# Kernel tuning notes

Hardware: AMD Instinct MI355X
Metric: run time of the kernel (lower is better)

Reference implementation:

```python
import jax, jax.numpy as jnp
import numpy as np

N, E, D, L, B, T = 50000, 600000, 128, 7, 512, 10
ATOM_DIMS = [119, 4, 12, 12, 10, 6, 6, 2, 2]
BOND_DIMS = [5, 6, 2]
MSG_EPS = 1e-7   # GENConv message epsilon
BN_EPS = 1e-5    # torch BatchNorm1d eps


def _offsets(dims):
    return jnp.asarray(np.concatenate([[0], np.cumsum(dims[:-1])]), dtype=jnp.int32)


def setup_inputs():
    key = jax.random.key(0)
    k = lambda i: jax.random.fold_in(key, i)
    x = jnp.stack([jax.random.randint(k(i), (N,), 0, d) for i, d in enumerate(ATOM_DIMS)], axis=1)
    edge_attr = jnp.stack([jax.random.randint(k(100 + i), (E,), 0, d) for i, d in enumerate(BOND_DIMS)], axis=1)
    edge_index = jax.random.randint(k(200), (2, E), 0, N)
    batch = jnp.sort(jax.random.randint(k(201), (N,), 0, B))
    atom_table = 0.1 * jax.random.normal(k(300), (sum(ATOM_DIMS), D), jnp.float32)
    bond_table = 0.1 * jax.random.normal(k(301), (sum(BOND_DIMS), D), jnp.float32)
    norm_gamma = jnp.ones((L, D), jnp.float32)
    norm_beta = jnp.zeros((L, D), jnp.float32)
    t = 0.1 * jnp.ones((L,), jnp.float32)
    mlp_w1 = 0.05 * jax.random.normal(k(302), (L, D, 2 * D), jnp.float32)
    mlp_b1 = jnp.zeros((L, 2 * D), jnp.float32)
    mlp_bng = jnp.ones((L, 2 * D), jnp.float32)
    mlp_bnb = jnp.zeros((L, 2 * D), jnp.float32)
    mlp_w2 = 0.05 * jax.random.normal(k(303), (L, 2 * D, D), jnp.float32)
    mlp_b2 = jnp.zeros((L, D), jnp.float32)
    pred_w = 0.05 * jax.random.normal(k(304), (D, T), jnp.float32)
    pred_b = jnp.zeros((T,), jnp.float32)
    return dict(x=x, edge_index=edge_index, edge_attr=edge_attr, batch=batch,
                atom_offsets=_offsets(ATOM_DIMS), bond_offsets=_offsets(BOND_DIMS),
                atom_table=atom_table, bond_table=bond_table,
                norm_gamma=norm_gamma, norm_beta=norm_beta, t=t,
                mlp_w1=mlp_w1, mlp_b1=mlp_b1, mlp_bng=mlp_bng, mlp_bnb=mlp_bnb,
                mlp_w2=mlp_w2, mlp_b2=mlp_b2, pred_w=pred_w, pred_b=pred_b)


def _batchnorm(z, gamma, beta):
    # training-mode BatchNorm1d: batch stats, biased variance
    mu = z.mean(0)
    var = z.var(0)
    return (z - mu) * jax.lax.rsqrt(var + BN_EPS) * gamma + beta


def _genconv(h, ea, src, dst, t, w1, b1, g1, bt1, w2, b2):
    # GENConv: message = relu(x_j + edge_attr) + eps; softmax aggregation with temperature t
    msg = jax.nn.relu(h[src] + ea) + MSG_EPS                 # [E, D]
    logits = msg * t
    m = jax.ops.segment_max(logits, dst, num_segments=N)     # [N, D]
    m = jax.lax.stop_gradient(jnp.where(jnp.isfinite(m), m, 0.0))
    e = jnp.exp(logits - m[dst])
    denom = jax.ops.segment_sum(e, dst, num_segments=N)
    alpha = e / (denom[dst] + 1e-16)
    aggr = jax.ops.segment_sum(msg * alpha, dst, num_segments=N)  # [N, D]
    out = h + aggr                                           # update: x_r + aggr
    z = _batchnorm(out @ w1 + b1, g1, bt1)                   # MLP: D -> 2D (BN, ReLU) -> D
    return jax.nn.relu(z) @ w2 + b2


def reference(x, edge_index, edge_attr, batch, atom_offsets, bond_offsets,
              atom_table, bond_table, norm_gamma, norm_beta, t,
              mlp_w1, mlp_b1, mlp_bng, mlp_bnb, mlp_w2, mlp_b2, pred_w, pred_b):
    h = atom_table[x + atom_offsets[None, :]].sum(1)               # [N, D] AtomEncoder
    ea = bond_table[edge_attr + bond_offsets[None, :]].sum(1)      # [E, D] BondEncoder
    src, dst = edge_index[0], edge_index[1]
    # first layer: bare conv
    h = _genconv(h, ea, src, dst, t[0], mlp_w1[0], mlp_b1[0], mlp_bng[0], mlp_bnb[0], mlp_w2[0], mlp_b2[0])
    # remaining layers: res+ blocks (norm -> act -> conv -> residual); dropout=0
    for i in range(1, L):
        r = jax.nn.relu(_batchnorm(h, norm_gamma[i], norm_beta[i]))
        r = _genconv(r, ea, src, dst, t[i], mlp_w1[i], mlp_b1[i], mlp_bng[i], mlp_bnb[i], mlp_w2[i], mlp_b2[i])
        h = h + r
    h = _batchnorm(h, norm_gamma[0], norm_beta[0])                 # layers[0].norm
    # global mean pool over graphs
    sums = jax.ops.segment_sum(h, batch, num_segments=B)
    cnts = jax.ops.segment_sum(jnp.ones((N,), h.dtype), batch, num_segments=B)
    graph_emb = sums / jnp.maximum(cnts, 1.0)[:, None]
    return graph_emb @ pred_w + pred_b                             # [B, T]
```

## Files before the change

### kernel.cpp

```cpp
#include <hip/hip_runtime.h>
#include <hip/hip_bf16.h>

#define N_NODES 50000
#define N_EDGES 600000
#define D 128
#define D2 256
#define NGRAPH 512
#define NTARGET 10
#define NSB 49
#define NSLOT 32

static constexpr float MSG_EPS_F = 1e-7f;
static constexpr float BN_EPS_F  = 1e-5f;

typedef _Float16 half8 __attribute__((ext_vector_type(8)));
typedef _Float16 half4v __attribute__((ext_vector_type(4)));
typedef float f32x4 __attribute__((ext_vector_type(4)));
#define MFMA16(a, b, c) __builtin_amdgcn_mfma_f32_16x16x32_f16(a, b, c, 0, 0, 0)

__global__ __launch_bounds__(256) void k_encode(
    const int* __restrict__ x, const int* __restrict__ aoff,
    const float* __restrict__ atab, float* __restrict__ h,
    _Float16* __restrict__ hh, int* __restrict__ deg) {
  int tid = blockIdx.x * 256 + threadIdx.x;
  if (tid < N_NODES) deg[tid] = 0;
  int n = tid >> 5, f4 = (tid & 31) << 2;
  if (n >= N_NODES) return;
  float4 acc = make_float4(0.f, 0.f, 0.f, 0.f);
#pragma unroll
  for (int i = 0; i < 9; ++i) {
    int row = x[n * 9 + i] + aoff[i];
    float4 v = *(const float4*)&atab[row * D + f4];
    acc.x += v.x; acc.y += v.y; acc.z += v.z; acc.w += v.w;
  }
  *(float4*)&h[(size_t)n * D + f4] = acc;
  half4v o = {(_Float16)acc.x, (_Float16)acc.y, (_Float16)acc.z, (_Float16)acc.w};
  *(half4v*)&hh[(size_t)n * D + f4] = o;
}

__global__ __launch_bounds__(128) void k_combo(
    const int* __restrict__ boff, const float* __restrict__ btab,
    _Float16* __restrict__ comboh) {
  int c = blockIdx.x, t = threadIdx.x;
  int a0 = c / 12, a1 = (c % 12) / 2, a2 = c % 2;
  comboh[c * D + t] = (_Float16)(btab[(boff[0] + a0) * D + t] +
                                 btab[(boff[1] + a1) * D + t] +
                                 btab[(boff[2] + a2) * D + t]);
}

__global__ __launch_bounds__(256) void k_packW(
    const float* __restrict__ w1, const float* __restrict__ w2,
    _Float16* __restrict__ w1p, _Float16* __restrict__ w2p) {
  int t = blockIdx.x * 256 + threadIdx.x;
  if (t < 7 * 4096) {
    int lane = t & 63, ntAll = (t >> 6) & 15, kc = (t >> 10) & 3, l = t >> 12;
    int q = lane >> 4, c = ntAll * 16 + (lane & 15);
    int kbase = kc * 32 + q * 8;
    const float* W = w1 + (size_t)l * D * D2;
    half8 v;
#pragma unroll
    for (int j = 0; j < 8; ++j) v[j] = (_Float16)W[(size_t)(kbase + j) * D2 + c];
    *(half8*)&w1p[(size_t)t * 8] = v;
  } else {
    int u = t - 7 * 4096;
    if (u < 7 * 4096) {
      int lane = u & 63, nt = (u >> 6) & 7, kcAll = (u >> 9) & 7, l = u >> 12;
      int q = lane >> 4, c = nt * 16 + (lane & 15);
      int kbase = kcAll * 32 + q * 8;
      const float* W = w2 + (size_t)l * D2 * D;
      half8 v;
#pragma unroll
      for (int j = 0; j < 8; ++j) v[j] = (_Float16)W[(size_t)(kbase + j) * D + c];
      *(half8*)&w2p[(size_t)u * 8] = v;
    }
  }
}

__global__ __launch_bounds__(256) void k_degree(
    const int* __restrict__ ei, int* __restrict__ deg) {
  int e = blockIdx.x * 256 + threadIdx.x;
  if (e >= N_EDGES) return;
  atomicAdd(&deg[ei[N_EDGES + e]], 1);
}

__global__ __launch_bounds__(1024) void k_scan1(
    const int* __restrict__ deg, int* __restrict__ excl, int* __restrict__ bsum) {
  __shared__ int tmp[1024];
  int t = threadIdx.x, i = blockIdx.x * 1024 + t;
  int v = (i < N_NODES) ? deg[i] : 0;
  tmp[t] = v;
  __syncthreads();
  for (int off = 1; off < 1024; off <<= 1) {
    int add = (t >= off) ? tmp[t - off] : 0;
    __syncthreads();
    tmp[t] += add;
    __syncthreads();
  }
  if (i < N_NODES) excl[i] = tmp[t] - v;
  if (t == 1023) bsum[blockIdx.x] = tmp[1023];
}

__global__ __launch_bounds__(64) void k_scan2(int* __restrict__ bsum) {
  __shared__ int s[64];
  int t = threadIdx.x;
  int v = (t < NSB) ? bsum[t] : 0;
  s[t] = v;
  __syncthreads();
  for (int off = 1; off < 64; off <<= 1) {
    int add = (t >= off) ? s[t - off] : 0;
    __syncthreads();
    s[t] += add;
    __syncthreads();
  }
  if (t < NSB) bsum[t] = s[t] - v;
}

__global__ __launch_bounds__(256) void k_scan3(
    const int* __restrict__ excl, const int* __restrict__ bsum,
    int* __restrict__ rowptr, int* __restrict__ cursor) {
  int i = blockIdx.x * 256 + threadIdx.x;
  if (i < N_NODES) {
    int v = excl[i] + bsum[i >> 10];
    rowptr[i] = v;
    cursor[i] = v;
  }
  if (i == N_NODES) rowptr[N_NODES] = N_EDGES;
}

__global__ __launch_bounds__(256) void k_scatter(
    const int* __restrict__ ei, const int* __restrict__ eattr,
    int* __restrict__ cursor, int* __restrict__ payload) {
  int e = blockIdx.x * 256 + threadIdx.x;
  if (e >= N_EDGES) return;
  int src = ei[e], dst = ei[N_EDGES + e];
  int cid = eattr[e * 3 + 0] * 12 + eattr[e * 3 + 1] * 2 + eattr[e * 3 + 2];
  int pos = atomicAdd(&cursor[dst], 1);
  payload[pos] = (src << 6) | cid;
}

__global__ __launch_bounds__(256) void k_gbounds(
    const int* __restrict__ batch, int* __restrict__ gstart) {
  int n = blockIdx.x * 256 + threadIdx.x;
  if (n >= N_NODES) return;
  int b0 = batch[n];
  int b1 = (n + 1 < N_NODES) ? batch[n + 1] : NGRAPH;
  for (int bb = b0 + 1; bb <= b1; ++bb) gstart[bb] = n + 1;
  if (n == 0)
    for (int bb = 0; bb <= b0; ++bb) gstart[bb] = 0;
}

__global__ __launch_bounds__(256) void k_layer1(
    const _Float16* __restrict__ hh, const int* __restrict__ rowptr,
    const int* __restrict__ payload, const _Float16* __restrict__ comboh,
    const float* __restrict__ tptr, int l,
    const float* __restrict__ statHsPrev,
    const float* __restrict__ gamma, const float* __restrict__ beta,
    const _Float16* __restrict__ w1p, const float* __restrict__ b1,
    _Float16* __restrict__ z1h, float* __restrict__ stat1s) {
  __shared__ __align__(16) _Float16 Af[512 * 8];
  __shared__ float bnA[128], bnB[128];
  int tid = threadIdx.x;
  int row0 = blockIdx.x * 32;
  int slot = blockIdx.x & (NSLOT - 1);
  float negcap;
  if (l > 0) {
    if (tid < 128) {
      float s = 0.f, sq = 0.f;
#pragma unroll
      for (int sl = 0; sl < NSLOT; ++sl) {
        s += statHsPrev[sl * 256 + tid];
        sq += statHsPrev[sl * 256 + 128 + tid];
      }
      const float invN = 1.0f / (float)N_NODES;
      float mu = s * invN, var = sq * invN - mu * mu;
      float isg = rsqrtf(var + BN_EPS_F) * gamma[tid];
      bnA[tid] = isg;
      bnB[tid] = beta[tid] - mu * isg;
    }
    negcap = 0.f;
  } else {
    if (tid < 128) { bnA[tid] = 1.f; bnB[tid] = 0.f; }
    negcap = -1e30f;
  }
  __syncthreads();
  float tv = tptr[l];
  int f8 = (tid & 15) << 3;

#pragma unroll
  for (int pass = 0; pass < 2; ++pass) {
    int dl = pass * 16 + (tid >> 4);
    int dst = row0 + dl;
    half8 v;
    if (dst < N_NODES) {
      float a[8], bb[8];
#pragma unroll
      for (int j = 0; j < 8; ++j) { a[j] = bnA[f8 + j]; bb[j] = bnB[f8 + j]; }
      int s = rowptr[dst], e = rowptr[dst + 1];
      float den[8], S[8];
#pragma unroll
      for (int j = 0; j < 8; ++j) { den[j] = 0.f; S[j] = 0.f; }
      int i = s;
      for (; i + 1 < e; i += 2) {
        int p0 = payload[i], p1 = payload[i + 1];
        half8 h0 = *(const half8*)&hh[(size_t)(p0 >> 6) * D + f8];
        half8 h1v = *(const half8*)&hh[(size_t)(p1 >> 6) * D + f8];
        half8 c0 = *(const half8*)&comboh[(p0 & 63) * D + f8];
        half8 c1 = *(const half8*)&comboh[(p1 & 63) * D + f8];
#pragma unroll
        for (int j = 0; j < 8; ++j) {
          float r0 = fmaxf(fmaf((float)h0[j], a[j], bb[j]), negcap);
          float r1 = fmaxf(fmaf((float)h1v[j], a[j], bb[j]), negcap);
          float m0 = fmaxf(r0 + (float)c0[j], 0.f) + MSG_EPS_F;
          float m1 = fmaxf(r1 + (float)c1[j], 0.f) + MSG_EPS_F;
          float e0 = __expf(m0 * tv), e1 = __expf(m1 * tv);
          den[j] += e0 + e1;
          S[j] += m0 * e0 + m1 * e1;
        }
      }
      if (i < e) {
        int p0 = payload[i];
        half8 h0 = *(const half8*)&hh[(size_t)(p0 >> 6) * D + f8];
        half8 c0 = *(const half8*)&comboh[(p0 & 63) * D + f8];
#pragma unroll
        for (int j = 0; j < 8; ++j) {
          float r0 = fmaxf(fmaf((float)h0[j], a[j], bb[j]), negcap);
          float m0 = fmaxf(r0 + (float)c0[j], 0.f) + MSG_EPS_F;
          float e0 = __expf(m0 * tv);
          den[j] += e0;
          S[j] += m0 * e0;
        }
      }
      half8 hd = *(const half8*)&hh[(size_t)dst * D + f8];
#pragma unroll
      for (int j = 0; j < 8; ++j) {
        float rd = fmaxf(fmaf((float)hd[j], a[j], bb[j]), negcap);
        v[j] = (_Float16)(rd + S[j] / (den[j] + 1e-16f));
      }
    } else {
#pragma unroll
      for (int j = 0; j < 8; ++j) v[j] = (_Float16)0.f;
    }
    int kc = f8 >> 5, q = (f8 >> 3) & 3, lrow = dl & 15;
    int fslot = (kc * 2 + pass) * 64 + q * 16 + lrow;
    *(half8*)&Af[fslot * 8] = v;
  }
  __syncthreads();

  int wv = tid >> 6, ln = tid & 63;
  f32x4 acc[2][4];
#pragma unroll
  for (int i = 0; i < 2; ++i)
#pragma unroll
    for (int j = 0; j < 4; ++j) acc[i][j] = (f32x4){0.f, 0.f, 0.f, 0.f};

#pragma unroll
  for (int kc = 0; kc < 4; ++kc) {
    half8 a0 = *(half8*)&Af[((kc * 2 + 0) * 64 + ln) * 8];
    half8 a1 = *(half8*)&Af[((kc * 2 + 1) * 64 + ln) * 8];
#pragma unroll
    for (int nt = 0; nt < 4; ++nt) {
      int ntAll = wv * 4 + nt;
      half8 b = *(const half8*)&w1p[((size_t)(kc * 16 + ntAll) * 64 + ln) * 8];
      acc[0][nt] = MFMA16(a0, b, acc[0][nt]);
      acc[1][nt] = MFMA16(a1, b, acc[1][nt]);
    }
  }
  int lq = ln >> 4, lc = ln & 15;
  float cs[4], cq[4];
#pragma unroll
  for (int nt = 0; nt < 4; ++nt) { cs[nt] = 0.f; cq[nt] = 0.f; }
#pragma unroll
  for (int nt = 0; nt < 4; ++nt) {
    int col = (wv * 4 + nt) * 16 + lc;
    float bias = b1[col];
#pragma unroll
    for (int mt = 0; mt < 2; ++mt) {
      int rbase = row0 + mt * 16 + lq * 4;
#pragma unroll
      for (int rg = 0; rg < 4; ++rg) {
        int row = rbase + rg;
        if (row < N_NODES) {
          float z = acc[mt][nt][rg] + bias;
          z1h[(size_t)row * D2 + col] = (_Float16)z;
          cs[nt] += z; cq[nt] += z * z;
        }
      }
    }
  }
#pragma unroll
  for (int nt = 0; nt < 4; ++nt) {
    float v = cs[nt], q = cq[nt];
    v += __shfl_xor(v, 16); v += __shfl_xor(v, 32);
    q += __shfl_xor(q, 16); q += __shfl_xor(q, 32);
    if (lq == 0) {
      int col = (wv * 4 + nt) * 16 + lc;
      atomicAdd(&stat1s[slot * 512 + col], v);
      atomicAdd(&stat1s[slot * 512 + 256 + col], q);
    }
  }
}

__global__ __launch_bounds__(256) void k_gemm2(
    const _Float16* __restrict__ z1h, const float* __restrict__ stat1s,
    const float* __restrict__ g1, const float* __restrict__ bt1,
    const _Float16* __restrict__ w2p, const float* __restrict__ b2,
    float* __restrict__ h, _Float16* __restrict__ hh, int residual,
    float* __restrict__ statHs) {
  __shared__ __align__(16) _Float16 Af[1024 * 8];
  __shared__ float s1[512];
  const float invN = 1.0f / (float)N_NODES;
  int tid = threadIdx.x;
  int row0 = blockIdx.x * 32;
  int slot = blockIdx.x & (NSLOT - 1);

#pragma unroll
  for (int jj = 0; jj < 2; ++jj) {
    int j = jj * 256 + tid;
    float a = 0.f;
#pragma unroll
    for (int s = 0; s < NSLOT; ++s) a += stat1s[s * 512 + j];
    s1[j] = a;
  }
  __syncthreads();

#pragma unroll
  for (int s0 = 0; s0 < 4; ++s0) {
    int s = s0 * 256 + tid;
    int kcAll = s >> 7, mt = (s >> 6) & 1, l2 = s & 63;
    int row = row0 + mt * 16 + (l2 & 15);
    int kb = kcAll * 32 + ((l2 >> 4) << 3);
    half8 v;
    if (row < N_NODES) {
      half8 z = *(const half8*)&z1h[(size_t)row * D2 + kb];
#pragma unroll
      for (int j = 0; j < 8; ++j) {
        float mu = s1[kb + j] * invN;
        float isg = rsqrtf(s1[256 + kb + j] * invN - mu * mu + BN_EPS_F) * g1[kb + j];
        v[j] = (_Float16)fmaxf(((float)z[j] - mu) * isg + bt1[kb + j], 0.f);
      }
    } else {
#pragma unroll
      for (int j = 0; j < 8; ++j) v[j] = (_Float16)0.f;
    }
    *(half8*)&Af[s * 8] = v;
  }
  __syncthreads();

  int wv = tid >> 6, ln = tid & 63;
  f32x4 acc[2][2];
#pragma unroll
  for (int i = 0; i < 2; ++i)
#pragma unroll
    for (int j = 0; j < 2; ++j) acc[i][j] = (f32x4){0.f, 0.f, 0.f, 0.f};

#pragma unroll
  for (int kcAll = 0; kcAll < 8; ++kcAll) {
    half8 a0 = *(half8*)&Af[((kcAll * 2 + 0) * 64 + ln) * 8];
    half8 a1 = *(half8*)&Af[((kcAll * 2 + 1) * 64 + ln) * 8];
#pragma unroll
    for (int nt = 0; nt < 2; ++nt) {
      half8 b = *(const half8*)&w2p[((size_t)(kcAll * 8 + wv * 2 + nt) * 64 + ln) * 8];
      acc[0][nt] = MFMA16(a0, b, acc[0][nt]);
      acc[1][nt] = MFMA16(a1, b, acc[1][nt]);
    }
  }
  int lq = ln >> 4, lc = ln & 15;
  float cs[2], cq[2];
#pragma unroll
  for (int nt = 0; nt < 2; ++nt) { cs[nt] = 0.f; cq[nt] = 0.f; }
#pragma unroll
  for (int nt = 0; nt < 2; ++nt) {
    int col = (wv * 2 + nt) * 16 + lc;
    float bias = b2[col];
#pragma unroll
    for (int mt = 0; mt < 2; ++mt) {
      int rbase = row0 + mt * 16 + lq * 4;
#pragma unroll
      for (int rg = 0; rg < 4; ++rg) {
        int row = rbase + rg;
        if (row < N_NODES) {
          float v = acc[mt][nt][rg] + bias;
          if (residual) v += h[(size_t)row * D + col];
          h[(size_t)row * D + col] = v;
          hh[(size_t)row * D + col] = (_Float16)v;
          cs[nt] += v; cq[nt] += v * v;
        }
      }
    }
  }
#pragma unroll
  for (int nt = 0; nt < 2; ++nt) {
    float v = cs[nt], q = cq[nt];
    v += __shfl_xor(v, 16); v += __shfl_xor(v, 32);
    q += __shfl_xor(q, 16); q += __shfl_xor(q, 32);
    if (lq == 0) {
      int col = (wv * 2 + nt) * 16 + lc;
      atomicAdd(&statHs[slot * 256 + col], v);
      atomicAdd(&statHs[slot * 256 + 128 + col], q);
    }
  }
}

__global__ __launch_bounds__(256) void k_poolpred(
    const float* __restrict__ h, const int* __restrict__ gstart,
    const float* __restrict__ statHs, const float* __restrict__ gamma,
    const float* __restrict__ beta, const float* __restrict__ pw,
    const float* __restrict__ pb, float* __restrict__ out) {
  __shared__ float sH[256];
  __shared__ float emb[128];
  __shared__ float4 red[256];
  int b = blockIdx.x, tid = threadIdx.x;
  {
    float a = 0.f;
#pragma unroll
    for (int s = 0; s < NSLOT; ++s) a += statHs[s * 256 + tid];
    sH[tid] = a;
  }
  int fl = (tid & 31) << 2, ns = tid >> 5;
  int gs = gstart[b], ge = gstart[b + 1];
  float4 acc = make_float4(0.f, 0.f, 0.f, 0.f);
  for (int n = gs + ns; n < ge; n += 8) {
    float4 v = *(const float4*)&h[(size_t)n * D + fl];
    acc.x += v.x; acc.y += v.y; acc.z += v.z; acc.w += v.w;
  }
  red[tid] = acc;
  __syncthreads();
  if (ns < 4) {
    float4 o = red[tid + 128];
    acc.x += o.x; acc.y += o.y; acc.z += o.z; acc.w += o.w;
    red[tid] = acc;
  }
  __syncthreads();
  if (ns < 2) {
    float4 o = red[tid + 64];
    acc.x += o.x; acc.y += o.y; acc.z += o.z; acc.w += o.w;
    red[tid] = acc;
  }
  __syncthreads();
  if (ns == 0) {
    float4 o = red[tid + 32];
    acc.x += o.x; acc.y += o.y; acc.z += o.z; acc.w += o.w;
    const float invN = 1.0f / (float)N_NODES;
    float inv = (ge > gs) ? 1.0f / (float)(ge - gs) : 0.f;
    float av[4] = {acc.x, acc.y, acc.z, acc.w};
#pragma unroll
    for (int j = 0; j < 4; ++j) {
      int k = fl + j;
      float mu = sH[k] * invN;
      float var = sH[D + k] * invN - mu * mu;
      emb[k] = (ge > gs)
          ? (av[j] * inv - mu) * rsqrtf(var + BN_EPS_F) * gamma[k] + beta[k]
          : 0.f;
    }
  }
  __syncthreads();
  if (tid < NTARGET) {
    float o = pb[tid];
    for (int k = 0; k < D; ++k) o += emb[k] * pw[k * NTARGET + tid];
    out[b * NTARGET + tid] = o;
  }
}

extern "C" void kernel_launch(void* const* d_in, const int* in_sizes, int n_in,
                              void* d_out, int out_size, void* d_ws, size_t ws_size,
                              hipStream_t stream) {
  const int* x      = (const int*)d_in[0];
  const int* ei     = (const int*)d_in[1];
  const int* eattr  = (const int*)d_in[2];
  const int* batch  = (const int*)d_in[3];
  const int* aoff   = (const int*)d_in[4];
  const int* boff   = (const int*)d_in[5];
  const float* atab = (const float*)d_in[6];
  const float* btab = (const float*)d_in[7];
  const float* ngam = (const float*)d_in[8];
  const float* nbet = (const float*)d_in[9];
  const float* tptr = (const float*)d_in[10];
  const float* w1   = (const float*)d_in[11];
  const float* b1   = (const float*)d_in[12];
  const float* bng  = (const float*)d_in[13];
  const float* bnb  = (const float*)d_in[14];
  const float* w2   = (const float*)d_in[15];
  const float* b2   = (const float*)d_in[16];
  const float* pw   = (const float*)d_in[17];
  const float* pb   = (const float*)d_in[18];
  float* out = (float*)d_out;

  float* ws = (float*)d_ws;
  const size_t ND = (size_t)N_NODES * D;
  float* h      = ws;
  _Float16* hh  = (_Float16*)(ws + 1 * ND);
  _Float16* z1h = (_Float16*)(ws + 2 * ND);
  float* statAll = ws + 3 * ND;
  float* stat1sAll = statAll;
  float* statHsAll = statAll + 7 * NSLOT * 512;
  float* comboF = statHsAll + 7 * NSLOT * 256;
  _Float16* comboh = (_Float16*)comboF;
  _Float16* w1p = (_Float16*)(comboF + 60 * D);
  _Float16* w2p = w1p + 7 * 32768;
  int* ibuf     = (int*)(w2p + 7 * 32768);
  int* rowptr   = ibuf;
  int* cursor   = rowptr + N_NODES + 1;
  int* deg      = cursor + N_NODES;
  int* payload  = deg + N_NODES;
  int* gstart   = payload + N_EDGES;
  int* excl     = gstart + NGRAPH + 1;
  int* bsum     = excl + N_NODES;

  const int nodeBlocks = (N_NODES * 32 + 255) / 256;
  const int edgeThreadBlocks = (N_EDGES + 255) / 256;
  const int nBlocks256 = (N_NODES + 255) / 256;
  const int gRows32 = (N_NODES + 31) / 32;

  (void)hipMemsetAsync(statAll, 0, (size_t)7 * NSLOT * (512 + 256) * sizeof(float), stream);
  k_encode<<<nodeBlocks, 256, 0, stream>>>(x, aoff, atab, h, hh, deg);
  k_combo<<<60, 128, 0, stream>>>(boff, btab, comboh);
  k_packW<<<(2 * 7 * 4096 + 255) / 256, 256, 0, stream>>>(w1, w2, w1p, w2p);
  k_gbounds<<<nBlocks256, 256, 0, stream>>>(batch, gstart);
  k_degree<<<edgeThreadBlocks, 256, 0, stream>>>(ei, deg);
  k_scan1<<<NSB, 1024, 0, stream>>>(deg, excl, bsum);
  k_scan2<<<1, 64, 0, stream>>>(bsum);
  k_scan3<<<(N_NODES + 256) / 256, 256, 0, stream>>>(excl, bsum, rowptr, cursor);
  k_scatter<<<edgeThreadBlocks, 256, 0, stream>>>(ei, eattr, cursor, payload);

  for (int l = 0; l < 7; ++l) {
    k_layer1<<<gRows32, 256, 0, stream>>>(
        hh, rowptr, payload, comboh, tptr, l,
        (l > 0) ? statHsAll + (size_t)(l - 1) * NSLOT * 256 : statHsAll,
        ngam + l * D, nbet + l * D,
        w1p + (size_t)l * 32768, b1 + l * D2, z1h,
        stat1sAll + (size_t)l * NSLOT * 512);
    k_gemm2<<<gRows32, 256, 0, stream>>>(
        z1h, stat1sAll + (size_t)l * NSLOT * 512, bng + l * D2, bnb + l * D2,
        w2p + (size_t)l * 32768, b2 + l * D, h, hh, l > 0 ? 1 : 0,
        statHsAll + (size_t)l * NSLOT * 256);
  }

  k_poolpred<<<NGRAPH, 256, 0, stream>>>(h, gstart,
                                         statHsAll + (size_t)6 * NSLOT * 256,
                                         ngam, nbet, pw, pb, out);
}
```

Before: 952.4 us.

## Split fused aggregation+GEMM1 and process nodes in degree-sorted order

The fused per-layer aggregation-plus-first-GEMM kernel is split into a standalone softmax-aggregation kernel, a BN-coefficient kernel, and a separate GEMM1 kernel that reads the aggregated features from a new fp16 buffer. Nodes are reordered by in-degree through a histogram, scan and scatter permutation, so the 16-lane groups within a wavefront handle destinations of similar degree. The goal is less divergence and load imbalance in the gather loop. In exchange, every layer does an extra round trip of an N×128 fp16 tensor through global memory and launches two more kernels.

New measurement: 870.5 us. 1.09x faster.

```diff
diff --git a/kernel.cpp b/kernel.cpp
--- a/kernel.cpp
+++ b/kernel.cpp
@@ -139,8 +139,10 @@
 }
 
 __global__ __launch_bounds__(256) void k_gbounds(
-    const int* __restrict__ batch, int* __restrict__ gstart) {
+    const int* __restrict__ batch, int* __restrict__ gstart,
+    int* __restrict__ hist) {
   int n = blockIdx.x * 256 + threadIdx.x;
+  if (n < 64) hist[n] = 0;
   if (n >= N_NODES) return;
   int b0 = batch[n];
   int b1 = (n + 1 < N_NODES) ? batch[n + 1] : NGRAPH;
@@ -149,100 +151,158 @@
     for (int bb = 0; bb <= b0; ++bb) gstart[bb] = 0;
 }
 
-__global__ __launch_bounds__(256) void k_layer1(
+__global__ __launch_bounds__(256) void k_hist(
+    const int* __restrict__ deg, int* __restrict__ hist) {
+  __shared__ int lh[64];
+  int tid = threadIdx.x;
+  if (tid < 64) lh[tid] = 0;
+  __syncthreads();
+  int n = blockIdx.x * 256 + tid;
+  if (n < N_NODES) atomicAdd(&lh[min(deg[n], 63)], 1);
+  __syncthreads();
+  if (tid < 64 && lh[tid]) atomicAdd(&hist[tid], lh[tid]);
+}
+
+__global__ __launch_bounds__(64) void k_scanhist(
+    const int* __restrict__ hist, int* __restrict__ cursor2) {
+  __shared__ int s[64];
+  int t = threadIdx.x;
+  int v = hist[t];
+  s[t] = v;
+  __syncthreads();
+  for (int off = 1; off < 64; off <<= 1) {
+    int add = (t >= off) ? s[t - off] : 0;
+    __syncthreads();
+    s[t] += add;
+    __syncthreads();
+  }
+  cursor2[t] = s[t] - v;
+}
+
+__global__ __launch_bounds__(256) void k_permscatter(
+    const int* __restrict__ deg, int* __restrict__ cursor2,
+    int* __restrict__ perm) {
+  __shared__ int lh[64], lbase[64];
+  int tid = threadIdx.x;
+  if (tid < 64) lh[tid] = 0;
+  __syncthreads();
+  int n = blockIdx.x * 256 + tid;
+  int b = -1, lpos = 0;
+  if (n < N_NODES) {
+    b = min(deg[n], 63);
+    lpos = atomicAdd(&lh[b], 1);
+  }
+  __syncthreads();
+  if (tid < 64 && lh[tid]) lbase[tid] = atomicAdd(&cursor2[tid], lh[tid]);
+  __syncthreads();
+  if (b >= 0) perm[lbase[b] + lpos] = n;
+}
+
+__global__ __launch_bounds__(128) void k_bncoef(
+    const float* __restrict__ statHsPrev, const float* __restrict__ gamma,
+    const float* __restrict__ beta, float* __restrict__ bncoef, int identity) {
+  int t = threadIdx.x;
+  if (identity) {
+    bncoef[t] = 1.f;
+    bncoef[128 + t] = 0.f;
+    return;
+  }
+  float s = 0.f, sq = 0.f;
+#pragma unroll
+  for (int sl = 0; sl < NSLOT; ++sl) {
+    s += statHsPrev[sl * 256 + t];
+    sq += statHsPrev[sl * 256 + 128 + t];
+  }
+  const float invN = 1.0f / (float)N_NODES;
+  float mu = s * invN, var = sq * invN - mu * mu;
+  float isg = rsqrtf(var + BN_EPS_F) * gamma[t];
+  bncoef[t] = isg;
+  bncoef[128 + t] = beta[t] - mu * isg;
+}
+
+__global__ __launch_bounds__(256) void k_aggrx(
     const _Float16* __restrict__ hh, const int* __restrict__ rowptr,
     const int* __restrict__ payload, const _Float16* __restrict__ comboh,
-    const float* __restrict__ tptr, int l,
-    const float* __restrict__ statHsPrev,
-    const float* __restrict__ gamma, const float* __restrict__ beta,
-    const _Float16* __restrict__ w1p, const float* __restrict__ b1,
-    _Float16* __restrict__ z1h, float* __restrict__ stat1s) {
+    const int* __restrict__ perm, const float* __restrict__ tptr, int l,
+    const float* __restrict__ bncoef, float negcap, _Float16* __restrict__ xh) {
+  int tid = blockIdx.x * 256 + threadIdx.x;
+  int gi = tid >> 4, f8 = (tid & 15) << 3;
+  if (gi >= N_NODES) return;
+  int dst = perm[gi];
+  float tv = tptr[l];
+  float a[8], bb[8];
+  *(float4*)&a[0] = *(const float4*)&bncoef[f8];
+  *(float4*)&a[4] = *(const float4*)&bncoef[f8 + 4];
+  *(float4*)&bb[0] = *(const float4*)&bncoef[128 + f8];
+  *(float4*)&bb[4] = *(const float4*)&bncoef[128 + f8 + 4];
+  int s = rowptr[dst], e = rowptr[dst + 1];
+  float den[8], S[8];
+#pragma unroll
+  for (int j = 0; j < 8; ++j) { den[j] = 0.f; S[j] = 0.f; }
+  int i = s;
+  for (; i + 1 < e; i += 2) {
+    int p0 = payload[i], p1 = payload[i + 1];
+    half8 h0 = *(const half8*)&hh[(size_t)(p0 >> 6) * D + f8];
+    half8 h1v = *(const half8*)&hh[(size_t)(p1 >> 6) * D + f8];
+    half8 c0 = *(const half8*)&comboh[(p0 & 63) * D + f8];
+    half8 c1 = *(const half8*)&comboh[(p1 & 63) * D + f8];
+#pragma unroll
+    for (int j = 0; j < 8; ++j) {
+      float r0 = fmaxf(fmaf((float)h0[j], a[j], bb[j]), negcap);
+      float r1 = fmaxf(fmaf((float)h1v[j], a[j], bb[j]), negcap);
+      float m0 = fmaxf(r0 + (float)c0[j], 0.f) + MSG_EPS_F;
+      float m1 = fmaxf(r1 + (float)c1[j], 0.f) + MSG_EPS_F;
+      float e0 = __expf(m0 * tv), e1 = __expf(m1 * tv);
+      den[j] += e0 + e1;
+      S[j] += m0 * e0 + m1 * e1;
+    }
+  }
+  if (i < e) {
+    int p0 = payload[i];
+    half8 h0 = *(const half8*)&hh[(size_t)(p0 >> 6) * D + f8];
+    half8 c0 = *(const half8*)&comboh[(p0 & 63) * D + f8];
+#pragma unroll
+    for (int j = 0; j < 8; ++j) {
+      float r0 = fmaxf(fmaf((float)h0[j], a[j], bb[j]), negcap);
+      float m0 = fmaxf(r0 + (float)c0[j], 0.f) + MSG_EPS_F;
+      float e0 = __expf(m0 * tv);
+      den[j] += e0;
+      S[j] += m0 * e0;
+    }
+  }
+  half8 hd = *(const half8*)&hh[(size_t)dst * D + f8];
+  half8 o;
+#pragma unroll
+  for (int j = 0; j < 8; ++j) {
+    float rd = fmaxf(fmaf((float)hd[j], a[j], bb[j]), negcap);
+    o[j] = (_Float16)(rd + S[j] / (den[j] + 1e-16f));
+  }
+  *(half8*)&xh[(size_t)dst * D + f8] = o;
+}
+
+__global__ __launch_bounds__(256) void k_gemm1(
+    const _Float16* __restrict__ xh, const _Float16* __restrict__ w1p,
+    const float* __restrict__ b1, _Float16* __restrict__ z1h,
+    float* __restrict__ stat1s) {
   __shared__ __align__(16) _Float16 Af[512 * 8];
-  __shared__ float bnA[128], bnB[128];
   int tid = threadIdx.x;
   int row0 = blockIdx.x * 32;
   int slot = blockIdx.x & (NSLOT - 1);
-  float negcap;
-  if (l > 0) {
-    if (tid < 128) {
-      float s = 0.f, sq = 0.f;
-#pragma unroll
-      for (int sl = 0; sl < NSLOT; ++sl) {
-        s += statHsPrev[sl * 256 + tid];
-        sq += statHsPrev[sl * 256 + 128 + tid];
-      }
-      const float invN = 1.0f / (float)N_NODES;
-      float mu = s * invN, var = sq * invN - mu * mu;
-      float isg = rsqrtf(var + BN_EPS_F) * gamma[tid];
-      bnA[tid] = isg;
-      bnB[tid] = beta[tid] - mu * isg;
-    }
-    negcap = 0.f;
-  } else {
-    if (tid < 128) { bnA[tid] = 1.f; bnB[tid] = 0.f; }
-    negcap = -1e30f;
-  }
-  __syncthreads();
-  float tv = tptr[l];
-  int f8 = (tid & 15) << 3;
-
-#pragma unroll
-  for (int pass = 0; pass < 2; ++pass) {
-    int dl = pass * 16 + (tid >> 4);
-    int dst = row0 + dl;
+
+#pragma unroll
+  for (int s0 = 0; s0 < 2; ++s0) {
+    int s = s0 * 256 + tid;
+    int kc = s >> 7, mt = (s >> 6) & 1, l2 = s & 63;
+    int row = row0 + mt * 16 + (l2 & 15);
+    int kb = kc * 32 + ((l2 >> 4) << 3);
     half8 v;
-    if (dst < N_NODES) {
-      float a[8], bb[8];
-#pragma unroll
-      for (int j = 0; j < 8; ++j) { a[j] = bnA[f8 + j]; bb[j] = bnB[f8 + j]; }
-      int s = rowptr[dst], e = rowptr[dst + 1];
-      float den[8], S[8];
-#pragma unroll
-      for (int j = 0; j < 8; ++j) { den[j] = 0.f; S[j] = 0.f; }
-      int i = s;
-      for (; i + 1 < e; i += 2) {
-        int p0 = payload[i], p1 = payload[i + 1];
-        half8 h0 = *(const half8*)&hh[(size_t)(p0 >> 6) * D + f8];
-        half8 h1v = *(const half8*)&hh[(size_t)(p1 >> 6) * D + f8];
-        half8 c0 = *(const half8*)&comboh[(p0 & 63) * D + f8];
-        half8 c1 = *(const half8*)&comboh[(p1 & 63) * D + f8];
-#pragma unroll
-        for (int j = 0; j < 8; ++j) {
-          float r0 = fmaxf(fmaf((float)h0[j], a[j], bb[j]), negcap);
-          float r1 = fmaxf(fmaf((float)h1v[j], a[j], bb[j]), negcap);
-          float m0 = fmaxf(r0 + (float)c0[j], 0.f) + MSG_EPS_F;
-          float m1 = fmaxf(r1 + (float)c1[j], 0.f) + MSG_EPS_F;
-          float e0 = __expf(m0 * tv), e1 = __expf(m1 * tv);
-          den[j] += e0 + e1;
-          S[j] += m0 * e0 + m1 * e1;
-        }
-      }
-      if (i < e) {
-        int p0 = payload[i];
-        half8 h0 = *(const half8*)&hh[(size_t)(p0 >> 6) * D + f8];
-        half8 c0 = *(const half8*)&comboh[(p0 & 63) * D + f8];
-#pragma unroll
-        for (int j = 0; j < 8; ++j) {
-          float r0 = fmaxf(fmaf((float)h0[j], a[j], bb[j]), negcap);
-          float m0 = fmaxf(r0 + (float)c0[j], 0.f) + MSG_EPS_F;
-          float e0 = __expf(m0 * tv);
-          den[j] += e0;
-          S[j] += m0 * e0;
-        }
-      }
-      half8 hd = *(const half8*)&hh[(size_t)dst * D + f8];
-#pragma unroll
-      for (int j = 0; j < 8; ++j) {
-        float rd = fmaxf(fmaf((float)hd[j], a[j], bb[j]), negcap);
-        v[j] = (_Float16)(rd + S[j] / (den[j] + 1e-16f));
-      }
+    if (row < N_NODES) {
+      v = *(const half8*)&xh[(size_t)row * D + kb];
     } else {
 #pragma unroll
       for (int j = 0; j < 8; ++j) v[j] = (_Float16)0.f;
     }
-    int kc = f8 >> 5, q = (f8 >> 3) & 3, lrow = dl & 15;
-    int fslot = (kc * 2 + pass) * 64 + q * 16 + lrow;
-    *(half8*)&Af[fslot * 8] = v;
+    *(half8*)&Af[s * 8] = v;
   }
   __syncthreads();
 
@@ -489,11 +549,13 @@
   const size_t ND = (size_t)N_NODES * D;
   float* h      = ws;
   _Float16* hh  = (_Float16*)(ws + 1 * ND);
+  _Float16* xh  = (_Float16*)(ws + 1 * ND + ND / 2);
   _Float16* z1h = (_Float16*)(ws + 2 * ND);
   float* statAll = ws + 3 * ND;
   float* stat1sAll = statAll;
   float* statHsAll = statAll + 7 * NSLOT * 512;
-  float* comboF = statHsAll + 7 * NSLOT * 256;
+  float* bncoef = statHsAll + 7 * NSLOT * 256;
+  float* comboF = bncoef + 256;
   _Float16* comboh = (_Float16*)comboF;
   _Float16* w1p = (_Float16*)(comboF + 60 * D);
   _Float16* w2p = w1p + 7 * 32768;
@@ -505,8 +567,12 @@
   int* gstart   = payload + N_EDGES;
   int* excl     = gstart + NGRAPH + 1;
   int* bsum     = excl + N_NODES;
+  int* hist     = bsum + 64;
+  int* cursor2  = hist + 64;
+  int* perm     = cursor2 + 64;
 
   const int nodeBlocks = (N_NODES * 32 + 255) / 256;
+  const int aggrBlocks = (N_NODES * 16 + 255) / 256;
   const int edgeThreadBlocks = (N_EDGES + 255) / 256;
   const int nBlocks256 = (N_NODES + 255) / 256;
   const int gRows32 = (N_NODES + 31) / 32;
@@ -515,20 +581,26 @@
   k_encode<<<nodeBlocks, 256, 0, stream>>>(x, aoff, atab, h, hh, deg);
   k_combo<<<60, 128, 0, stream>>>(boff, btab, comboh);
   k_packW<<<(2 * 7 * 4096 + 255) / 256, 256, 0, stream>>>(w1, w2, w1p, w2p);
-  k_gbounds<<<nBlocks256, 256, 0, stream>>>(batch, gstart);
+  k_gbounds<<<nBlocks256, 256, 0, stream>>>(batch, gstart, hist);
   k_degree<<<edgeThreadBlocks, 256, 0, stream>>>(ei, deg);
   k_scan1<<<NSB, 1024, 0, stream>>>(deg, excl, bsum);
   k_scan2<<<1, 64, 0, stream>>>(bsum);
   k_scan3<<<(N_NODES + 256) / 256, 256, 0, stream>>>(excl, bsum, rowptr, cursor);
   k_scatter<<<edgeThreadBlocks, 256, 0, stream>>>(ei, eattr, cursor, payload);
+  k_hist<<<nBlocks256, 256, 0, stream>>>(deg, hist);
+  k_scanhist<<<1, 64, 0, stream>>>(hist, cursor2);
+  k_permscatter<<<nBlocks256, 256, 0, stream>>>(deg, cursor2, perm);
 
   for (int l = 0; l < 7; ++l) {
-    k_layer1<<<gRows32, 256, 0, stream>>>(
-        hh, rowptr, payload, comboh, tptr, l,
+    k_bncoef<<<1, 128, 0, stream>>>(
         (l > 0) ? statHsAll + (size_t)(l - 1) * NSLOT * 256 : statHsAll,
-        ngam + l * D, nbet + l * D,
-        w1p + (size_t)l * 32768, b1 + l * D2, z1h,
-        stat1sAll + (size_t)l * NSLOT * 512);
+        ngam + l * D, nbet + l * D, bncoef, l == 0 ? 1 : 0);
+    k_aggrx<<<aggrBlocks, 256, 0, stream>>>(
+        hh, rowptr, payload, comboh, perm, tptr, l, bncoef,
+        l == 0 ? -1e30f : 0.f, xh);
+    k_gemm1<<<gRows32, 256, 0, stream>>>(xh, w1p + (size_t)l * 32768,
+                                         b1 + l * D2, z1h,
+                                         stat1sAll + (size_t)l * NSLOT * 512);
     k_gemm2<<<gRows32, 256, 0, stream>>>(
         z1h, stat1sAll + (size_t)l * NSLOT * 512, bng + l * D2, bnb + l * D2,
         w2p + (size_t)l * 32768, b2 + l * D, h, hh, l > 0 ? 1 : 0,
```
